# Performance work log

Hardware: AMD Instinct MI355X
Metric: run time of the kernel (lower is better)

The kernel has to match this reference:

```python
import jax, jax.numpy as jnp
import numpy as np

B, T, D = 128, 2048, 256


def setup_inputs() -> dict:
    key = jax.random.key(0)
    ks = jax.random.split(key, 6)
    s = 1.0 / np.sqrt(D)  # kaiming-uniform-ish scale for bias-free Linear
    return {
        "x": jax.random.normal(ks[0], (B, T, D), jnp.float32),
        "W_in": jax.random.normal(ks[1], (D, D), jnp.float32) * s,
        "W_select": jax.random.normal(ks[2], (D, D), jnp.float32) * s,
        "W_gate": jax.random.normal(ks[3], (D, D), jnp.float32) * s,
        "W_out": jax.random.normal(ks[4], (D, D), jnp.float32) * s,
        "W_delta": jax.random.normal(ks[5], (D, D), jnp.float32) * s,
        "log_a": jnp.zeros((D,), jnp.float32),  # module inits log_a = zeros
    }


def _diag_recurrence(decay, update):
    # state_t = decay_t * state_{t-1} + update_t, state_{-1} = 0 (zero-init fast path)
    # First-order linear recurrence as an associative scan:
    # (a1,b1) o (a2,b2) = (a1*a2, a2*b1 + b2)
    def combine(c1, c2):
        a1, b1 = c1
        a2, b2 = c2
        return a1 * a2, a2 * b1 + b2

    _, states = jax.lax.associative_scan(combine, (decay, update), axis=1)
    return states  # (B, T, D)


def reference(x, W_in, W_select, W_gate, W_out, W_delta, log_a):
    # selective diag-SSM (a_mode='diag'):
    #   delta  = softplus(delta_proj(x))                  timestep / selectivity
    #   decay  = exp(-delta * exp(log_a))                 in (0, 1]
    #   update = delta * sigmoid(select_proj(x)) * in_proj(x)
    #   states = scan(state = decay*state + update)
    #   y      = states * silu(gate_proj(x)); out = out_proj(y)
    delta = jax.nn.softplus(jnp.einsum("btd,ed->bte", x, W_delta))
    decay = jnp.exp(-delta * jnp.exp(log_a))
    u = jnp.einsum("btd,ed->bte", x, W_in)
    sel = jax.nn.sigmoid(jnp.einsum("btd,ed->bte", x, W_select))
    update = delta * sel * u
    states = _diag_recurrence(decay, update)
    gate = jax.nn.silu(jnp.einsum("btd,ed->bte", x, W_gate))
    return jnp.einsum("btd,ed->bte", states * gate, W_out)
```

## Files before the change

kernel.cpp:

```cpp
#include <hip/hip_runtime.h>
#include <hip/hip_bf16.h>
#include <hip/hip_fp16.h>
#include <math.h>


typedef __attribute__((ext_vector_type(8))) short s16x8;
typedef __attribute__((ext_vector_type(4))) float f32x4;

#define D_DIM 256
#define T_DIM 2048
#define B_DIM 128
#define NCHUNK 16
#define CLEN 128
#define BK 64

__device__ __forceinline__ unsigned short f2bf(float f) {
    union { float f; unsigned int u; } v; v.f = f;
    unsigned int r = v.u + 0x7fffu + ((v.u >> 16) & 1u);
    return (unsigned short)(r >> 16);
}
__device__ __forceinline__ float bf2f(unsigned short s) {
    union { unsigned int u; float f; } v; v.u = ((unsigned int)s) << 16;
    return v.f;
}
__device__ __forceinline__ void gload_lds16(const void* g, void* l) {
    __builtin_amdgcn_global_load_lds(
        (const __attribute__((address_space(1))) unsigned int*)g,
        (__attribute__((address_space(3))) unsigned int*)l, 16, 0, 0);
}

__global__ __launch_bounds__(256) void prep_kernel(
    const float* __restrict__ W_in, const float* __restrict__ W_select,
    const float* __restrict__ W_gate, const float* __restrict__ W_out,
    const float* __restrict__ W_delta, const float* __restrict__ log_a,
    unsigned short* __restrict__ Wb, float* __restrict__ ea)
{
    int i = blockIdx.x * 256 + threadIdx.x;
    if (i < 4 * 65536) {
        int row = i >> 8, k = i & 255;
        int n = row >> 2, w = row & 3;
        const float* src = (w == 0) ? W_delta : (w == 1) ? W_select
                         : (w == 2) ? W_in    : W_gate;
        Wb[i] = f2bf(src[n * 256 + k]);
    } else if (i < 5 * 65536) {
        Wb[i] = f2bf(W_out[i - 4 * 65536]);
    } else if (i < 5 * 65536 + 256) {
        int j = i - 5 * 65536;
        ea[j] = expf(log_a[j]);
    }
}

__global__ __launch_bounds__(256) void xcast_kernel(
    const float* __restrict__ x, unsigned short* __restrict__ xb)
{
    size_t i = ((size_t)blockIdx.x * 256 + threadIdx.x) * 8;
    float4 p0 = *(const float4*)(x + i);
    float4 p1 = *(const float4*)(x + i + 4);
    s16x8 a;
    a[0] = (short)f2bf(p0.x); a[1] = (short)f2bf(p0.y);
    a[2] = (short)f2bf(p0.z); a[3] = (short)f2bf(p0.w);
    a[4] = (short)f2bf(p1.x); a[5] = (short)f2bf(p1.y);
    a[6] = (short)f2bf(p1.z); a[7] = (short)f2bf(p1.w);
    *(s16x8*)(xb + i) = a;
}

__global__ __launch_bounds__(256, 2) void gemm_fused_kernel(
    const unsigned short* __restrict__ xb, const unsigned short* __restrict__ Wcat,
    const float* __restrict__ ea,
    __half2* __restrict__ du, unsigned short* __restrict__ gate,
    float* __restrict__ cA, float* __restrict__ cS)
{
    __shared__ char ldsb[65536];
    int bid = blockIdx.x;
    int wg  = (bid & 7) * 2048 + (bid >> 3);
    int mt  = wg >> 3;
    int nt  = wg & 7;
    int mbase = mt * 128;
    int nb = nt * 128;
    int tid = threadIdx.x, lane = tid & 63, wid = tid >> 6;
    int l16 = lane & 15, lk = lane >> 4;
    int wr = wid >> 1, wc = wid & 1;
    int srow = tid >> 3;
    int sgi  = tid & 7;

    f32x4 acc[4][4] = {};

    {
        int kb = 0;
#pragma unroll
        for (int j = 0; j < 4; ++j) {
            int row = j * 32 + srow;
            int sg  = sgi ^ (row & 7);
            gload_lds16(xb + (size_t)(mbase + row) * D_DIM + kb + sg * 8,
                        ldsb + row * 128 + sgi * 16);
            gload_lds16(Wcat + (size_t)(nb + row) * D_DIM + kb + sg * 8,
                        ldsb + 16384 + row * 128 + sgi * 16);
        }
    }
    __syncthreads();

    for (int ks = 0; ks < 4; ++ks) {
        int bufo = (ks & 1) << 15;
        if (ks < 3) {
            int kb = (ks + 1) * BK;
            int nbo = bufo ^ 32768;
#pragma unroll
            for (int j = 0; j < 4; ++j) {
                int row = j * 32 + srow;
                int sg  = sgi ^ (row & 7);
                gload_lds16(xb + (size_t)(mbase + row) * D_DIM + kb + sg * 8,
                            ldsb + nbo + row * 128 + sgi * 16);
                gload_lds16(Wcat + (size_t)(nb + row) * D_DIM + kb + sg * 8,
                            ldsb + nbo + 16384 + row * 128 + sgi * 16);
            }
        }
#pragma unroll
        for (int kk = 0; kk < 2; ++kk) {
            int gp = ((kk * 4 + lk) ^ (l16 & 7)) * 16;
            s16x8 xf[4], wf[4];
#pragma unroll
            for (int mf = 0; mf < 4; ++mf)
                xf[mf] = *(const s16x8*)(ldsb + bufo
                           + (wr * 64 + mf * 16 + l16) * 128 + gp);
#pragma unroll
            for (int nf = 0; nf < 4; ++nf)
                wf[nf] = *(const s16x8*)(ldsb + bufo + 16384
                           + (wc * 64 + nf * 16 + l16) * 128 + gp);
#pragma unroll
            for (int nf = 0; nf < 4; ++nf)
#pragma unroll
                for (int mf = 0; mf < 4; ++mf)
                    acc[mf][nf] = __builtin_amdgcn_mfma_f32_16x16x32_bf16(
                        wf[nf], xf[mf], acc[mf][nf], 0, 0, 0);
        }
        if (ks < 3) __syncthreads();
    }

    __half2* scanb = (__half2*)ldsb;
    float2*  sums  = (float2*)(ldsb + 16384);
#pragma unroll
    for (int nf = 0; nf < 4; ++nf) {
        int n = nt * 32 + wc * 16 + nf * 4 + lk;
        float ean = ea[n];
        int dl = wc * 16 + nf * 4 + lk;
        int cxor = (dl & 7) << 2;
#pragma unroll
        for (int mf = 0; mf < 4; ++mf) {
            int t = wr * 64 + mf * 16 + l16;
            int m = mbase + t;
            float zd = acc[mf][nf][0];
            float zs = acc[mf][nf][1];
            float zi = acc[mf][nf][2];
            float zg = acc[mf][nf][3];
            float e = __expf(zd);
            float delta = (zd > 15.f) ? zd : __logf(1.f + e);
            float dec = __expf(-delta * ean);
            float sel = 1.f / (1.f + __expf(-zs));
            float upd = delta * sel * zi;
            float g   = zg / (1.f + __expf(-zg));
            __half2 dv = __floats2half2_rn(dec, upd);
            du[(size_t)m * D_DIM + n] = dv;
            gate[(size_t)m * D_DIM + n] = f2bf(g);
            scanb[dl * 128 + (t ^ cxor)] = dv;
        }
    }
    __syncthreads();

    {
        int dloc = tid & 31, sub = tid >> 5;
        int cxor = (dloc & 7) << 2;
        float A = 1.f, S = 0.f;
        int t0 = sub * 16;
#pragma unroll 4
        for (int i = 0; i < 16; ++i) {
            int t = t0 + i;
            __half2 v = scanb[dloc * 128 + (t ^ cxor)];
            float dc = __low2float(v), up = __high2float(v);
            A *= dc;
            S = fmaf(dc, S, up);
        }
        sums[sub * 32 + dloc] = make_float2(A, S);
    }
    __syncthreads();
    if (tid < 32) {
        float A = 1.f, S = 0.f;
#pragma unroll
        for (int sub = 0; sub < 8; ++sub) {
            float2 as = sums[sub * 32 + tid];
            S = fmaf(as.x, S, as.y);
            A *= as.x;
        }
        int idx = mt * D_DIM + nt * 32 + tid;
        cA[idx] = A;
        cS[idx] = S;
    }
}

__global__ __launch_bounds__(256) void scan2_kernel(
    const float* __restrict__ cA, const float* __restrict__ cS,
    float* __restrict__ carry)
{
    int b = blockIdx.x;
    int d = threadIdx.x;
    float s = 0.f;
    for (int c = 0; c < NCHUNK; ++c) {
        int idx = (b * NCHUNK + c) * D_DIM + d;
        carry[idx] = s;
        s = fmaf(cA[idx], s, cS[idx]);
    }
}

__global__ __launch_bounds__(256) void scan_out_kernel(
    const __half2* __restrict__ du, const unsigned short* __restrict__ gate,
    const float* __restrict__ carry, const unsigned short* __restrict__ Wo,
    float* __restrict__ out)
{
    __shared__ unsigned short yls[128 * 256];
    int b = blockIdx.x >> 4;
    int c = blockIdx.x & 15;
    int tid = threadIdx.x;

    {
        int d = tid;
        size_t base = ((size_t)b * T_DIM + (size_t)c * CLEN) * D_DIM + d;
        float s = carry[(b * NCHUNK + c) * D_DIM + d];
        int dlo = d & 7, dch = d >> 3;
#pragma unroll 4
        for (int t = 0; t < CLEN; ++t) {
            __half2 v = du[base + (size_t)t * D_DIM];
            float dc = __low2float(v);
            float up = __high2float(v);
            s = fmaf(dc, s, up);
            float g = bf2f(gate[base + (size_t)t * D_DIM]);
            int off = t * 256 + ((dch ^ (t & 7)) << 3) + dlo;
            yls[off] = f2bf(s * g);
        }
    }
    __syncthreads();

    int lane = tid & 63, wid = tid >> 6;
    int l16 = lane & 15;
    int lkc = lane >> 4;
    int m0 = (wid >> 1) * 64;
    size_t rbase = (size_t)b * T_DIM + (size_t)c * CLEN;
    int r0 = lkc * 4;

    for (int nblk = 0; nblk < 2; ++nblk) {
        int n0 = (wid & 1) * 64 + nblk * 128;
        f32x4 acc[4][4] = {};
        for (int ks = 0; ks < 8; ++ks) {
            int kb = ks * 32 + lkc * 8;
            s16x8 yf[4];
#pragma unroll
            for (int mf = 0; mf < 4; ++mf) {
                int row = m0 + mf * 16 + l16;
                int chunk = (ks * 4 + lkc) ^ (row & 7);
                yf[mf] = *(const s16x8*)&yls[row * 256 + chunk * 8];
            }
#pragma unroll
            for (int nf = 0; nf < 4; ++nf) {
                s16x8 wfr = *(const s16x8*)(Wo + (size_t)(n0 + nf * 16 + l16) * D_DIM + kb);
#pragma unroll
                for (int mf = 0; mf < 4; ++mf)
                    acc[mf][nf] = __builtin_amdgcn_mfma_f32_16x16x32_bf16(
                        wfr, yf[mf], acc[mf][nf], 0, 0, 0);
            }
        }
#pragma unroll
        for (int mf = 0; mf < 4; ++mf) {
            size_t rowg = rbase + m0 + mf * 16 + l16;
#pragma unroll
            for (int nf = 0; nf < 4; ++nf) {
                int n = n0 + nf * 16 + r0;
                *(f32x4*)(out + rowg * D_DIM + n) = acc[mf][nf];
            }
        }
    }
}

extern "C" void kernel_launch(void* const* d_in, const int* in_sizes, int n_in,
                              void* d_out, int out_size, void* d_ws, size_t ws_size,
                              hipStream_t stream)
{
    const float* x        = (const float*)d_in[0];
    const float* W_in     = (const float*)d_in[1];
    const float* W_select = (const float*)d_in[2];
    const float* W_gate   = (const float*)d_in[3];
    const float* W_out    = (const float*)d_in[4];
    const float* W_delta  = (const float*)d_in[5];
    const float* log_a    = (const float*)d_in[6];
    float* out = (float*)d_out;

    char* ws = (char*)d_ws;
    const size_t MB = 1ull << 20;
    unsigned short* Wb    = (unsigned short*)(ws);
    float*          ea    = (float*)(ws + 655360);
    unsigned short* xb    = (unsigned short*)(ws + 1 * MB);
    __half2*        du    = (__half2*)(ws + 129 * MB);
    unsigned short* gate  = (unsigned short*)(ws + 385 * MB);
    float*          cA    = (float*)(ws + 513 * MB);
    float*          cS    = (float*)(ws + 515 * MB);
    float*          carry = (float*)(ws + 517 * MB);

    prep_kernel<<<1281, 256, 0, stream>>>(W_in, W_select, W_gate, W_out,
                                          W_delta, log_a, Wb, ea);
    xcast_kernel<<<32768, 256, 0, stream>>>(x, xb);
    gemm_fused_kernel<<<16384, 256, 0, stream>>>(xb, Wb, ea, du, gate, cA, cS);
    scan2_kernel<<<B_DIM, 256, 0, stream>>>(cA, cS, carry);
    scan_out_kernel<<<B_DIM * NCHUNK, 256, 0, stream>>>(du, gate, carry,
                                                        Wb + 4 * 65536, out);
}
```

Before: 673.7 us.

## Fuse x fp32-to-bf16 cast into GEMM, load fp32 directly into LDS

```diff
diff --git a/kernel.cpp b/kernel.cpp
--- a/kernel.cpp
+++ b/kernel.cpp
@@ -22,6 +22,16 @@
 __device__ __forceinline__ float bf2f(unsigned short s) {
     union { unsigned int u; float f; } v; v.u = ((unsigned int)s) << 16;
     return v.f;
+}
+__device__ __forceinline__ s16x8 cvt2(float4 p0, float4 p1) {
+    union { __hip_bfloat162 h; unsigned int u; } c0, c1, c2, c3;
+    c0.h = __float22bfloat162_rn({p0.x, p0.y});
+    c1.h = __float22bfloat162_rn({p0.z, p0.w});
+    c2.h = __float22bfloat162_rn({p1.x, p1.y});
+    c3.h = __float22bfloat162_rn({p1.z, p1.w});
+    union { unsigned int u[4]; s16x8 v; } r;
+    r.u[0] = c0.u; r.u[1] = c1.u; r.u[2] = c2.u; r.u[3] = c3.u;
+    return r.v;
 }
 __device__ __forceinline__ void gload_lds16(const void* g, void* l) {
     __builtin_amdgcn_global_load_lds(
@@ -50,27 +60,13 @@
     }
 }
 
-__global__ __launch_bounds__(256) void xcast_kernel(
-    const float* __restrict__ x, unsigned short* __restrict__ xb)
-{
-    size_t i = ((size_t)blockIdx.x * 256 + threadIdx.x) * 8;
-    float4 p0 = *(const float4*)(x + i);
-    float4 p1 = *(const float4*)(x + i + 4);
-    s16x8 a;
-    a[0] = (short)f2bf(p0.x); a[1] = (short)f2bf(p0.y);
-    a[2] = (short)f2bf(p0.z); a[3] = (short)f2bf(p0.w);
-    a[4] = (short)f2bf(p1.x); a[5] = (short)f2bf(p1.y);
-    a[6] = (short)f2bf(p1.z); a[7] = (short)f2bf(p1.w);
-    *(s16x8*)(xb + i) = a;
-}
-
-__global__ __launch_bounds__(256, 2) void gemm_fused_kernel(
-    const unsigned short* __restrict__ xb, const unsigned short* __restrict__ Wcat,
+__global__ __launch_bounds__(256, 3) void gemm_fused_kernel(
+    const float* __restrict__ x, const unsigned short* __restrict__ Wcat,
     const float* __restrict__ ea,
     __half2* __restrict__ du, unsigned short* __restrict__ gate,
     float* __restrict__ cA, float* __restrict__ cS)
 {
-    __shared__ char ldsb[65536];
+    __shared__ char ldsb[49152];
     int bid = blockIdx.x;
     int wg  = (bid & 7) * 2048 + (bid >> 3);
     int mt  = wg >> 3;
@@ -80,51 +76,45 @@
     int tid = threadIdx.x, lane = tid & 63, wid = tid >> 6;
     int l16 = lane & 15, lk = lane >> 4;
     int wr = wid >> 1, wc = wid & 1;
-    int srow = tid >> 3;
-    int sgi  = tid & 7;
 
     f32x4 acc[4][4] = {};
 
-    {
-        int kb = 0;
+    for (int ks = 0; ks < 4; ++ks) {
+        int kb = ks * BK;
+#pragma unroll
+        for (int j = 0; j < 8; ++j) {
+            int e = j * 256 + tid;
+            int row = e >> 4, gsl = e & 15;
+            int g = gsl ^ (row & 7);
+            gload_lds16(x + (size_t)(mbase + row) * D_DIM + kb + g * 4,
+                        ldsb + e * 16);
+        }
 #pragma unroll
         for (int j = 0; j < 4; ++j) {
-            int row = j * 32 + srow;
-            int sg  = sgi ^ (row & 7);
-            gload_lds16(xb + (size_t)(mbase + row) * D_DIM + kb + sg * 8,
-                        ldsb + row * 128 + sgi * 16);
-            gload_lds16(Wcat + (size_t)(nb + row) * D_DIM + kb + sg * 8,
-                        ldsb + 16384 + row * 128 + sgi * 16);
-        }
-    }
-    __syncthreads();
-
-    for (int ks = 0; ks < 4; ++ks) {
-        int bufo = (ks & 1) << 15;
-        if (ks < 3) {
-            int kb = (ks + 1) * BK;
-            int nbo = bufo ^ 32768;
-#pragma unroll
-            for (int j = 0; j < 4; ++j) {
-                int row = j * 32 + srow;
-                int sg  = sgi ^ (row & 7);
-                gload_lds16(xb + (size_t)(mbase + row) * D_DIM + kb + sg * 8,
-                            ldsb + nbo + row * 128 + sgi * 16);
-                gload_lds16(Wcat + (size_t)(nb + row) * D_DIM + kb + sg * 8,
-                            ldsb + nbo + 16384 + row * 128 + sgi * 16);
-            }
-        }
+            int e = j * 256 + tid;
+            int row = e >> 3, gsl = e & 7;
+            int g = gsl ^ (row & 7);
+            gload_lds16(Wcat + (size_t)(nb + row) * D_DIM + kb + g * 8,
+                        ldsb + 32768 + e * 16);
+        }
+        __syncthreads();
+
 #pragma unroll
         for (int kk = 0; kk < 2; ++kk) {
+            s16x8 xf[4], wf[4];
+#pragma unroll
+            for (int mf = 0; mf < 4; ++mf) {
+                int rowA = wr * 64 + mf * 16 + l16;
+                int s = rowA & 7;
+                int g0 = kk * 8 + lk * 2;
+                float4 a0 = *(const float4*)(ldsb + rowA * 256 + ((g0 ^ s) * 16));
+                float4 a1 = *(const float4*)(ldsb + rowA * 256 + (((g0 + 1) ^ s) * 16));
+                xf[mf] = cvt2(a0, a1);
+            }
             int gp = ((kk * 4 + lk) ^ (l16 & 7)) * 16;
-            s16x8 xf[4], wf[4];
-#pragma unroll
-            for (int mf = 0; mf < 4; ++mf)
-                xf[mf] = *(const s16x8*)(ldsb + bufo
-                           + (wr * 64 + mf * 16 + l16) * 128 + gp);
 #pragma unroll
             for (int nf = 0; nf < 4; ++nf)
-                wf[nf] = *(const s16x8*)(ldsb + bufo + 16384
+                wf[nf] = *(const s16x8*)(ldsb + 32768
                            + (wc * 64 + nf * 16 + l16) * 128 + gp);
 #pragma unroll
             for (int nf = 0; nf < 4; ++nf)
@@ -133,17 +123,16 @@
                     acc[mf][nf] = __builtin_amdgcn_mfma_f32_16x16x32_bf16(
                         wf[nf], xf[mf], acc[mf][nf], 0, 0, 0);
         }
-        if (ks < 3) __syncthreads();
+        __syncthreads();
     }
 
     __half2* scanb = (__half2*)ldsb;
-    float2*  sums  = (float2*)(ldsb + 16384);
+    float2*  sums  = (float2*)(ldsb + 20480);
 #pragma unroll
     for (int nf = 0; nf < 4; ++nf) {
         int n = nt * 32 + wc * 16 + nf * 4 + lk;
         float ean = ea[n];
         int dl = wc * 16 + nf * 4 + lk;
-        int cxor = (dl & 7) << 2;
 #pragma unroll
         for (int mf = 0; mf < 4; ++mf) {
             int t = wr * 64 + mf * 16 + l16;
@@ -161,20 +150,18 @@
             __half2 dv = __floats2half2_rn(dec, upd);
             du[(size_t)m * D_DIM + n] = dv;
             gate[(size_t)m * D_DIM + n] = f2bf(g);
-            scanb[dl * 128 + (t ^ cxor)] = dv;
+            scanb[dl * 129 + t] = dv;
         }
     }
     __syncthreads();
 
     {
         int dloc = tid & 31, sub = tid >> 5;
-        int cxor = (dloc & 7) << 2;
         float A = 1.f, S = 0.f;
         int t0 = sub * 16;
 #pragma unroll 4
         for (int i = 0; i < 16; ++i) {
-            int t = t0 + i;
-            __half2 v = scanb[dloc * 128 + (t ^ cxor)];
+            __half2 v = scanb[dloc * 129 + t0 + i];
             float dc = __low2float(v), up = __high2float(v);
             A *= dc;
             S = fmaf(dc, S, up);
@@ -295,17 +282,15 @@
     const size_t MB = 1ull << 20;
     unsigned short* Wb    = (unsigned short*)(ws);
     float*          ea    = (float*)(ws + 655360);
-    unsigned short* xb    = (unsigned short*)(ws + 1 * MB);
-    __half2*        du    = (__half2*)(ws + 129 * MB);
-    unsigned short* gate  = (unsigned short*)(ws + 385 * MB);
-    float*          cA    = (float*)(ws + 513 * MB);
-    float*          cS    = (float*)(ws + 515 * MB);
-    float*          carry = (float*)(ws + 517 * MB);
+    __half2*        du    = (__half2*)(ws + 1 * MB);
+    unsigned short* gate  = (unsigned short*)(ws + 257 * MB);
+    float*          cA    = (float*)(ws + 385 * MB);
+    float*          cS    = (float*)(ws + 387 * MB);
+    float*          carry = (float*)(ws + 389 * MB);
 
     prep_kernel<<<1281, 256, 0, stream>>>(W_in, W_select, W_gate, W_out,
                                           W_delta, log_a, Wb, ea);
-    xcast_kernel<<<32768, 256, 0, stream>>>(x, xb);
-    gemm_fused_kernel<<<16384, 256, 0, stream>>>(xb, Wb, ea, du, gate, cA, cS);
+    gemm_fused_kernel<<<16384, 256, 0, stream>>>(x, Wb, ea, du, gate, cA, cS);
     scan2_kernel<<<B_DIM, 256, 0, stream>>>(cA, cS, carry);
     scan_out_kernel<<<B_DIM * NCHUNK, 256, 0, stream>>>(du, gate, carry,
                                                         Wb + 4 * 65536, out);
```

Result: faster. 647.0 us (-4.0%).
